# Optimization experiments

Measured on AMD Instinct MI355X. Metric: run time of the kernel, lower is better.

The kernel has to match this reference:

```python
import jax, jax.numpy as jnp
import numpy as np

NU, MS, DT, R = 128, 64, 128, 4
D_, K_, B_ = 10.0, 0.3, 0.3  # Layer1 sigmoid-gain hyperparams (LBKT defaults)


def setup_inputs() -> dict:
    key = jax.random.key(0)
    ks = jax.random.split(key, 16)
    B = 4096
    glorot = lambda k, shape: jax.random.normal(k, shape, jnp.float32) * np.sqrt(2.0 / (shape[-2] + shape[-1]))
    return {
        "inputs": jax.random.uniform(ks[0], (B, NU + MS + DT + 3), jnp.float32),
        "states": jax.random.normal(ks[1], (1, B, MS, NU), jnp.float32),
        "time_weight": glorot(ks[2], (R, NU + 1, NU)),
        "attempt_weight": glorot(ks[3], (R, NU + 1, NU)),
        "hint_weight": glorot(ks[4], (R, NU + 1, NU)),
        "Wf": glorot(ks[5], (1, R)),
        "bias": glorot(ks[6], (1, NU)),
        "gate3_W": glorot(ks[7], (2 * NU + 150, NU)),
        "gate3_b": jnp.zeros((NU,), jnp.float32),
        "out_W": glorot(ks[8], (NU + DT, NU)),
        "out_b": jnp.zeros((NU,), jnp.float32),
        "tg_W": glorot(ks[9], (2 * NU, NU)),
        "tg_b": jnp.zeros((1, NU), jnp.float32),
        "ag_W": glorot(ks[10], (2 * NU, NU)),
        "ag_b": jnp.zeros((1, NU), jnp.float32),
        "hg_W": glorot(ks[11], (2 * NU, NU)),
        "hg_b": jnp.zeros((1, NU), jnp.float32),
    }


def reference(inputs, states, time_weight, attempt_weight, hint_weight, Wf, bias,
              gate3_W, gate3_b, out_W, out_b, tg_W, tg_b, ag_W, ag_b, hg_W, hg_b):
    interact_emb = inputs[:, :NU]                       # (B, NU)
    corr = inputs[:, NU:NU + MS]                        # (B, MS) correlation weights
    topic = inputs[:, NU + MS:NU + MS + DT]             # (B, DT)
    t_f = inputs[:, -3:-2]                              # (B, 1)
    a_f = inputs[:, -2:-1]
    h_f = inputs[:, -1:]
    h_pre = states[0]                                   # (B, MS, NU)

    # correlation-weighted memory read
    h_pre_tilde = jnp.einsum('bm,bmn->bn', corr, h_pre)

    out_layer = lambda x: jax.nn.sigmoid(x @ out_W + out_b)
    preds = out_layer(jnp.concatenate([h_pre_tilde, topic], -1)).sum(-1, keepdims=True) / NU

    # Layer1 behavior-gain sub-networks: sigmoid(linear([h_tilde, interact]) * gain(factor))
    hx = jnp.concatenate([h_pre_tilde, interact_emb], -1)  # (B, 2*NU)
    def layer1(factor, W, b):
        gain = K_ + (1.0 - K_) / (1.0 + jnp.exp(-D_ * (factor - B_)))  # (B,1)
        return jax.nn.sigmoid((hx @ W + b) * gain)

    time_gain = layer1(t_f, tg_W, tg_b)
    attempt_gain = layer1(a_f, ag_W, ag_b)
    hint_gain = layer1(h_f, hg_W, hg_b)

    # low-rank tensor fusion: append a ones column, contract against (R, NU+1, NU)
    pad = jnp.ones_like(t_f)
    fuse = lambda g, W: jnp.einsum('bu,run->rbn', jnp.concatenate([g, pad], -1), W)
    fusion_all = fuse(time_gain, time_weight) * fuse(attempt_gain, attempt_weight) * fuse(hint_gain, hint_weight)
    fusion_all = jnp.einsum('or,rbn->bn', Wf, fusion_all) + bias  # (B, NU)
    learning_gain = jax.nn.relu(fusion_all)

    # outer-product write over memory slots
    LG = corr[:, :, None] * learning_gain[:, None, :]   # (B, MS, NU)

    Bsz = inputs.shape[0]
    tile50 = lambda f: jnp.broadcast_to(f[:, None, :], (Bsz, MS, 50))
    gate_in = jnp.concatenate([
        h_pre,
        jnp.broadcast_to(interact_emb[:, None, :], (Bsz, MS, NU)),
        tile50(t_f), tile50(a_f), tile50(h_f),
    ], -1)                                              # (B, MS, 2*NU+150)
    forget_gate = jax.nn.sigmoid(gate_in @ gate3_W + gate3_b)

    h = h_pre * forget_gate + LG                        # dropout inactive (inference)
    h_tilde = jnp.einsum('bm,bmn->bn', corr, h)
    after_preds = out_layer(jnp.concatenate([h_tilde, topic], -1)).sum(-1, keepdims=True) / NU
    improve = (after_preds - preds) / (1.0 - preds)
    result = jnp.concatenate([preds, improve], -1)      # (B, 2)
    return result, h
```

## Files before the change

### kernel.cpp

```cpp
#include <hip/hip_runtime.h>

#define B_TOT 4096
#define IN_W 323

typedef __attribute__((ext_vector_type(8))) short short8;
typedef __attribute__((ext_vector_type(4))) float f32x4;
typedef unsigned short ushort_t;

#define MFMA16(a, b, c) __builtin_amdgcn_mfma_f32_16x16x32_bf16(a, b, c, 0, 0, 0)

__device__ __forceinline__ float sigmoidf_(float x) { return 1.0f / (1.0f + __expf(-x)); }

__device__ __forceinline__ ushort_t f2bf(float f) {
    unsigned int u = __float_as_uint(f);
    u += 0x7FFF + ((u >> 16) & 1);
    return (ushort_t)(u >> 16);
}

union BF8 { ushort_t u[8]; short8 v; };

struct WS {
    ushort_t *hpt, *ieb, *topb, *gains, *htldb;
    ushort_t *oWb, *tgWb, *agWb, *hgWb, *g3W2b, *W1b, *fWb;
    float *wsum, *preds, *cvec, *lg;
};

__global__ __launch_bounds__(256) void k0_prep(
    const float* __restrict__ inp, const float* __restrict__ oW,
    const float* __restrict__ tgW, const float* __restrict__ agW, const float* __restrict__ hgW,
    const float* __restrict__ g3W, const float* __restrict__ tw, const float* __restrict__ aw,
    const float* __restrict__ hw, WS w) {
    int bx = blockIdx.x, tid = threadIdx.x;
    if (bx < 128) {
        int mat = bx >> 5, c = bx & 31;
        const float* src = mat == 0 ? oW : mat == 1 ? tgW : mat == 2 ? agW : hgW;
        ushort_t* dst = mat == 0 ? w.oWb : mat == 1 ? w.tgWb : mat == 2 ? w.agWb : w.hgWb;
        if (tid < 128) {
            int n = tid;
#pragma unroll
            for (int j = 0; j < 8; ++j)
                dst[(size_t)n * 256 + c * 8 + j] = f2bf(src[(size_t)(c * 8 + j) * 128 + n]);
        }
    } else if (bx < 352) {
        int i = bx - 128, mat = i >> 4, c = i & 15;
        const float* src;
        ushort_t* dst;
        if (mat == 0) { src = g3W + 128 * 128; dst = w.g3W2b; }
        else if (mat == 1) { src = g3W; dst = w.W1b; }
        else {
            int f = mat - 2, g = f >> 2, r = f & 3;
            const float* base = g == 0 ? tw : g == 1 ? aw : hw;
            src = base + (size_t)r * 129 * 128;
            dst = w.fWb + (size_t)f * 128 * 128;
        }
        if (tid < 128) {
            int n = tid;
#pragma unroll
            for (int j = 0; j < 8; ++j)
                dst[(size_t)n * 128 + c * 8 + j] = f2bf(src[(size_t)(c * 8 + j) * 128 + n]);
        }
    } else if (bx == 352) {
        if (tid < 128) {
            int n = tid;
            float st = 0.f, sa = 0.f, sh = 0.f;
            for (int k = 0; k < 50; ++k) {
                st += g3W[(size_t)(256 + k) * 128 + n];
                sa += g3W[(size_t)(306 + k) * 128 + n];
                sh += g3W[(size_t)(356 + k) * 128 + n];
            }
            w.wsum[n] = st; w.wsum[128 + n] = sa; w.wsum[256 + n] = sh;
        }
    } else {
        int id0 = (bx - 353) * 256 + tid;
        for (int id = id0; id < 2 * B_TOT * 128; id += 1024 * 256) {
            int arr = id >> 19;
            int rem = id & 524287;
            int b = rem >> 7, n = rem & 127;
            float v = inp[(size_t)b * IN_W + (arr ? 192 : 0) + n];
            (arr ? w.topb : w.ieb)[rem] = f2bf(v);
        }
    }
}

__global__ __launch_bounds__(256) void k1a_hpt(const float* __restrict__ inp,
                                               const float* __restrict__ hp, WS w) {
    __shared__ float s_corr[8][64];
    int tid = threadIdx.x, b0 = blockIdx.x * 8;
    for (int i = tid; i < 512; i += 256) {
        int bl = i >> 6, m = i & 63;
        s_corr[bl][m] = inp[(size_t)(b0 + bl) * IN_W + 128 + m];
    }
    __syncthreads();
    int bl = tid >> 5, c4 = (tid & 31) * 4;
    const float* hpb = hp + (size_t)(b0 + bl) * 8192 + c4;
    float a0 = 0, a1 = 0, a2 = 0, a3 = 0;
#pragma unroll 8
    for (int m = 0; m < 64; ++m) {
        float cr = s_corr[bl][m];
        float4 v = *(const float4*)(hpb + m * 128);
        a0 += cr * v.x; a1 += cr * v.y; a2 += cr * v.z; a3 += cr * v.w;
    }
    ushort_t* dst = w.hpt + (size_t)(b0 + bl) * 128 + c4;
    dst[0] = f2bf(a0); dst[1] = f2bf(a1); dst[2] = f2bf(a2); dst[3] = f2bf(a3);
}

__global__ __launch_bounds__(256) void k1b_gemms(
    const float* __restrict__ inp, const float* __restrict__ ob,
    const float* __restrict__ tgb, const float* __restrict__ agb, const float* __restrict__ hgb,
    const float* __restrict__ g3b, WS w) {
    __shared__ float s_red[4][16];
    int tid = threadIdx.x;
    int job = blockIdx.y;
    int m0 = blockIdx.x * 16;
    int wv = tid >> 6, l = tid & 63;
    int lr = l & 15, lg_ = l >> 4;
    int ncol0 = wv * 32;
    const ushort_t* Bw = job == 0 ? w.oWb : job == 1 ? w.tgWb : job == 2 ? w.agWb
                         : job == 3 ? w.hgWb : w.g3W2b;
    const int K = (job == 4) ? 128 : 256;
    f32x4 acc0 = {0, 0, 0, 0}, acc1 = {0, 0, 0, 0};
    for (int k0 = 0; k0 < K; k0 += 32) {
        const ushort_t* Ab;
        int ka;
        if (job == 4) { Ab = w.ieb; ka = k0; }
        else if (k0 < 128) { Ab = w.hpt; ka = k0; }
        else { Ab = (job == 0) ? w.topb : w.ieb; ka = k0 - 128; }
        short8 a = *(const short8*)(Ab + (size_t)(m0 + lr) * 128 + ka + lg_ * 8);
        short8 b0v = *(const short8*)(Bw + (size_t)(ncol0 + lr) * K + k0 + lg_ * 8);
        short8 b1v = *(const short8*)(Bw + (size_t)(ncol0 + 16 + lr) * K + k0 + lg_ * 8);
        acc0 = MFMA16(a, b0v, acc0);
        acc1 = MFMA16(a, b1v, acc1);
    }
    if (job == 0) {
        float s[4];
#pragma unroll
        for (int rr = 0; rr < 4; ++rr)
            s[rr] = sigmoidf_(acc0[rr] + ob[ncol0 + lr]) + sigmoidf_(acc1[rr] + ob[ncol0 + 16 + lr]);
#pragma unroll
        for (int off = 1; off <= 8; off <<= 1)
#pragma unroll
            for (int rr = 0; rr < 4; ++rr) s[rr] += __shfl_xor(s[rr], off);
        if (lr == 0)
#pragma unroll
            for (int rr = 0; rr < 4; ++rr) s_red[wv][lg_ * 4 + rr] = s[rr];
        __syncthreads();
        if (tid < 16) {
            float p = (s_red[0][tid] + s_red[1][tid] + s_red[2][tid] + s_red[3][tid]) * (1.f / 128.f);
            w.preds[m0 + tid] = p;
        }
    } else if (job <= 3) {
        const float* gb = job == 1 ? tgb : job == 2 ? agb : hgb;
        ushort_t* gout = w.gains + (size_t)(job - 1) * B_TOT * 128;
#pragma unroll
        for (int half = 0; half < 2; ++half) {
            f32x4 acc = half ? acc1 : acc0;
            int n = ncol0 + half * 16 + lr;
            float gbn = gb[n];
#pragma unroll
            for (int rr = 0; rr < 4; ++rr) {
                int b = m0 + lg_ * 4 + rr;
                float f = inp[(size_t)b * IN_W + 320 + (job - 1)];
                float gf = 0.3f + 0.7f * sigmoidf_(10.f * (f - 0.3f));
                gout[(size_t)b * 128 + n] = f2bf(sigmoidf_((acc[rr] + gbn) * gf));
            }
        }
    } else {
#pragma unroll
        for (int half = 0; half < 2; ++half) {
            f32x4 acc = half ? acc1 : acc0;
            int n = ncol0 + half * 16 + lr;
            float wst = w.wsum[n], wsa = w.wsum[128 + n], wsh = w.wsum[256 + n];
            float gbn = g3b[n];
#pragma unroll
            for (int rr = 0; rr < 4; ++rr) {
                int b = m0 + lg_ * 4 + rr;
                const float* sp = inp + (size_t)b * IN_W + 320;
                w.cvec[(size_t)b * 128 + n] = acc[rr] + sp[0] * wst + sp[1] * wsa + sp[2] * wsh + gbn;
            }
        }
    }
}

__global__ __launch_bounds__(512) void k1c_fusion(
    const float* __restrict__ tw, const float* __restrict__ aw, const float* __restrict__ hw,
    const float* __restrict__ wf, const float* __restrict__ bias, WS w) {
    __shared__ float s_red[4][16][128];
    int tid = threadIdx.x;
    int m0 = blockIdx.x * 16;
    int wv = tid >> 6, l = tid & 63;
    int r = wv >> 1, nh = wv & 1;
    int lr = l & 15, lg_ = l >> 4;
    f32x4 acc[3][4];
#pragma unroll
    for (int g = 0; g < 3; ++g)
#pragma unroll
        for (int nt = 0; nt < 4; ++nt) acc[g][nt] = (f32x4){0, 0, 0, 0};
#pragma unroll
    for (int g = 0; g < 3; ++g) {
        const ushort_t* Ag = w.gains + (size_t)g * B_TOT * 128;
        const ushort_t* Bg = w.fWb + (size_t)(g * 4 + r) * 128 * 128;
#pragma unroll
        for (int k0 = 0; k0 < 128; k0 += 32) {
            short8 a = *(const short8*)(Ag + (size_t)(m0 + lr) * 128 + k0 + lg_ * 8);
#pragma unroll
            for (int nt = 0; nt < 4; ++nt) {
                short8 b = *(const short8*)(Bg + (size_t)(nh * 64 + nt * 16 + lr) * 128 + k0 + lg_ * 8);
                acc[g][nt] = MFMA16(a, b, acc[g][nt]);
            }
        }
    }
    float wfr = wf[r];
    const float* pad0 = tw + (size_t)(r * 129 + 128) * 128;
    const float* pad1 = aw + (size_t)(r * 129 + 128) * 128;
    const float* pad2 = hw + (size_t)(r * 129 + 128) * 128;
#pragma unroll
    for (int nt = 0; nt < 4; ++nt) {
        int n = nh * 64 + nt * 16 + lr;
        float p0 = pad0[n], p1 = pad1[n], p2 = pad2[n];
#pragma unroll
        for (int rr = 0; rr < 4; ++rr) {
            float F0 = acc[0][nt][rr] + p0;
            float F1 = acc[1][nt][rr] + p1;
            float F2 = acc[2][nt][rr] + p2;
            s_red[r][lg_ * 4 + rr][n] = wfr * F0 * F1 * F2;
        }
    }
    __syncthreads();
    for (int i = tid; i < 2048; i += 512) {
        int row = i >> 7, col = i & 127;
        float v = s_red[0][row][col] + s_red[1][row][col] + s_red[2][row][col] + s_red[3][row][col];
        w.lg[(size_t)(m0 + row) * 128 + col] = fmaxf(v + bias[col], 0.f);
    }
}

__global__ __launch_bounds__(256) void k2_big(const float* __restrict__ inp,
                                              const float* __restrict__ hp, WS w,
                                              float* __restrict__ out_h) {
    __shared__ __align__(16) ushort_t s_w1[128 * 136];
    __shared__ float s_corr[64], s_lg[128], s_cv[128], s_ht[4][128];
    int tid = threadIdx.x, b = blockIdx.x;
    for (int i = tid; i < 128 * 16; i += 256) {
        int row = i >> 4, c8 = (i & 15) * 8;
        *(short8*)(s_w1 + row * 136 + c8) = *(const short8*)(w.W1b + (size_t)row * 128 + c8);
    }
    if (tid < 64) s_corr[tid] = inp[(size_t)b * IN_W + 128 + tid];
    if (tid < 128) s_lg[tid] = w.lg[(size_t)b * 128 + tid];
    else if (tid < 256) { int t = tid - 128; s_cv[t] = w.cvec[(size_t)b * 128 + t]; }
    __syncthreads();
    int wv = tid >> 6, l = tid & 63;
    int lr = l & 15, lg_ = l >> 4;
    int m0 = wv * 16;
    const float* hpb = hp + (size_t)b * 8192;
    short8 afr[4];
#pragma unroll
    for (int k0i = 0; k0i < 4; ++k0i) {
        const float* p = hpb + (m0 + lr) * 128 + k0i * 32 + lg_ * 8;
        float4 x0 = *(const float4*)p, x1 = *(const float4*)(p + 4);
        BF8 t;
        t.u[0] = f2bf(x0.x); t.u[1] = f2bf(x0.y); t.u[2] = f2bf(x0.z); t.u[3] = f2bf(x0.w);
        t.u[4] = f2bf(x1.x); t.u[5] = f2bf(x1.y); t.u[6] = f2bf(x1.z); t.u[7] = f2bf(x1.w);
        afr[k0i] = t.v;
    }
    float* outb = out_h + (size_t)b * 8192;
#pragma unroll
    for (int nt = 0; nt < 8; ++nt) {
        f32x4 acc = {0, 0, 0, 0};
#pragma unroll
        for (int k0i = 0; k0i < 4; ++k0i) {
            short8 bv = *(const short8*)(s_w1 + (nt * 16 + lr) * 136 + k0i * 32 + lg_ * 8);
            acc = MFMA16(afr[k0i], bv, acc);
        }
        int n = nt * 16 + lr;
        float cv = s_cv[n], lgv = s_lg[n];
        float csum = 0.f;
#pragma unroll
        for (int rr = 0; rr < 4; ++rr) {
            int m = m0 + lg_ * 4 + rr;
            float fg = sigmoidf_(acc[rr] + cv);
            float hpv = hpb[m * 128 + n];
            float cr = s_corr[m];
            float hv = hpv * fg + cr * lgv;
            outb[m * 128 + n] = hv;
            csum += cr * hv;
        }
        csum += __shfl_xor(csum, 16);
        csum += __shfl_xor(csum, 32);
        if (l < 16) s_ht[wv][n] = csum;
    }
    __syncthreads();
    if (tid < 128) {
        float s = s_ht[0][tid] + s_ht[1][tid] + s_ht[2][tid] + s_ht[3][tid];
        w.htldb[(size_t)b * 128 + tid] = f2bf(s);
    }
}

__global__ __launch_bounds__(256) void k3_after(const float* __restrict__ ob, WS w,
                                               float* __restrict__ out_res) {
    __shared__ float s_red[4][16];
    int tid = threadIdx.x, m0 = blockIdx.x * 16;
    int wv = tid >> 6, l = tid & 63, lr = l & 15, lg_ = l >> 4;
    int ncol0 = wv * 32;
    f32x4 acc0 = {0, 0, 0, 0}, acc1 = {0, 0, 0, 0};
    for (int k0 = 0; k0 < 256; k0 += 32) {
        const ushort_t* Ab = (k0 < 128) ? w.htldb : w.topb;
        int ka = k0 & 127;
        short8 a = *(const short8*)(Ab + (size_t)(m0 + lr) * 128 + ka + lg_ * 8);
        short8 b0v = *(const short8*)(w.oWb + (size_t)(ncol0 + lr) * 256 + k0 + lg_ * 8);
        short8 b1v = *(const short8*)(w.oWb + (size_t)(ncol0 + 16 + lr) * 256 + k0 + lg_ * 8);
        acc0 = MFMA16(a, b0v, acc0);
        acc1 = MFMA16(a, b1v, acc1);
    }
    float s[4];
#pragma unroll
    for (int rr = 0; rr < 4; ++rr)
        s[rr] = sigmoidf_(acc0[rr] + ob[ncol0 + lr]) + sigmoidf_(acc1[rr] + ob[ncol0 + 16 + lr]);
#pragma unroll
    for (int off = 1; off <= 8; off <<= 1)
#pragma unroll
        for (int rr = 0; rr < 4; ++rr) s[rr] += __shfl_xor(s[rr], off);
    if (lr == 0)
#pragma unroll
        for (int rr = 0; rr < 4; ++rr) s_red[wv][lg_ * 4 + rr] = s[rr];
    __syncthreads();
    if (tid < 16) {
        float ap = (s_red[0][tid] + s_red[1][tid] + s_red[2][tid] + s_red[3][tid]) * (1.f / 128.f);
        float p = w.preds[m0 + tid];
        out_res[(size_t)(m0 + tid) * 2] = p;
        out_res[(size_t)(m0 + tid) * 2 + 1] = (ap - p) / (1.f - p);
    }
}

extern "C" void kernel_launch(void* const* d_in, const int* in_sizes, int n_in,
                              void* d_out, int out_size, void* d_ws, size_t ws_size,
                              hipStream_t stream) {
    const float* inp  = (const float*)d_in[0];
    const float* st   = (const float*)d_in[1];
    const float* tw   = (const float*)d_in[2];
    const float* aw   = (const float*)d_in[3];
    const float* hw   = (const float*)d_in[4];
    const float* wf   = (const float*)d_in[5];
    const float* bias = (const float*)d_in[6];
    const float* g3W  = (const float*)d_in[7];
    const float* g3b  = (const float*)d_in[8];
    const float* oW   = (const float*)d_in[9];
    const float* ob   = (const float*)d_in[10];
    const float* tgW  = (const float*)d_in[11];
    const float* tgb  = (const float*)d_in[12];
    const float* agW  = (const float*)d_in[13];
    const float* agb  = (const float*)d_in[14];
    const float* hgW  = (const float*)d_in[15];
    const float* hgb  = (const float*)d_in[16];

    float* out_res = (float*)d_out;
    float* out_h   = (float*)d_out + 2 * B_TOT;

    char* p = (char*)d_ws;
    auto alloc = [&](size_t bytes) { char* r = p; p += (bytes + 255) & ~255ull; return r; };
    WS w;
    w.hpt   = (ushort_t*)alloc((size_t)B_TOT * 128 * 2);
    w.ieb   = (ushort_t*)alloc((size_t)B_TOT * 128 * 2);
    w.topb  = (ushort_t*)alloc((size_t)B_TOT * 128 * 2);
    w.gains = (ushort_t*)alloc((size_t)3 * B_TOT * 128 * 2);
    w.htldb = (ushort_t*)alloc((size_t)B_TOT * 128 * 2);
    w.oWb   = (ushort_t*)alloc(256 * 128 * 2);
    w.tgWb  = (ushort_t*)alloc(256 * 128 * 2);
    w.agWb  = (ushort_t*)alloc(256 * 128 * 2);
    w.hgWb  = (ushort_t*)alloc(256 * 128 * 2);
    w.g3W2b = (ushort_t*)alloc(128 * 128 * 2);
    w.W1b   = (ushort_t*)alloc(128 * 128 * 2);
    w.fWb   = (ushort_t*)alloc(12 * 128 * 128 * 2);
    w.wsum  = (float*)alloc(3 * 128 * 4);
    w.preds = (float*)alloc(B_TOT * 4);
    w.cvec  = (float*)alloc((size_t)B_TOT * 128 * 4);
    w.lg    = (float*)alloc((size_t)B_TOT * 128 * 4);

    k0_prep<<<1377, 256, 0, stream>>>(inp, oW, tgW, agW, hgW, g3W, tw, aw, hw, w);
    k1a_hpt<<<B_TOT / 8, 256, 0, stream>>>(inp, st, w);
    k1b_gemms<<<dim3(B_TOT / 16, 5), 256, 0, stream>>>(inp, ob, tgb, agb, hgb, g3b, w);
    k1c_fusion<<<B_TOT / 16, 512, 0, stream>>>(tw, aw, hw, wf, bias, w);
    k2_big<<<B_TOT, 256, 0, stream>>>(inp, st, w, out_h);
    k3_after<<<B_TOT / 16, 256, 0, stream>>>(ob, w, out_res);
}
```

Measured before the change: 356.1 us.

## Fuse stage-one kernels into one block-local pass and batch memory-update blocks

Merges the memory read, the gain/pred/gate GEMMs and the fusion GEMM into a single kernel. Intermediates (h_tilde, embeddings, gains) now stay in shared memory instead of round-tripping through global bf16 buffers. The weight prep kernel now transposes through shared memory with coalesced loads. The big update kernel processes four samples per block, one per wave, so the W1 tile staged in shared memory is reused across samples. The after kernel converts topic values from the inputs inline. The trade-off is fewer, heavier blocks with more serial MFMA work per wave and higher shared-memory use.

```diff
diff --git a/kernel.cpp b/kernel.cpp
--- a/kernel.cpp
+++ b/kernel.cpp
@@ -5,61 +5,32 @@
 
 typedef __attribute__((ext_vector_type(8))) short short8;
 typedef __attribute__((ext_vector_type(4))) float f32x4;
-typedef unsigned short ushort_t;
+typedef unsigned short u16;
 
 #define MFMA16(a, b, c) __builtin_amdgcn_mfma_f32_16x16x32_bf16(a, b, c, 0, 0, 0)
 
 __device__ __forceinline__ float sigmoidf_(float x) { return 1.0f / (1.0f + __expf(-x)); }
 
-__device__ __forceinline__ ushort_t f2bf(float f) {
+__device__ __forceinline__ u16 f2bf(float f) {
     unsigned int u = __float_as_uint(f);
     u += 0x7FFF + ((u >> 16) & 1);
-    return (ushort_t)(u >> 16);
-}
-
-union BF8 { ushort_t u[8]; short8 v; };
+    return (u16)(u >> 16);
+}
+
+union BF8 { u16 u[8]; short8 v; };
 
 struct WS {
-    ushort_t *hpt, *ieb, *topb, *gains, *htldb;
-    ushort_t *oWb, *tgWb, *agWb, *hgWb, *g3W2b, *W1b, *fWb;
+    u16 *oWb, *tgWb, *agWb, *hgWb, *g3W2b, *W1b, *fWb, *htldb;
     float *wsum, *preds, *cvec, *lg;
 };
 
 __global__ __launch_bounds__(256) void k0_prep(
-    const float* __restrict__ inp, const float* __restrict__ oW,
-    const float* __restrict__ tgW, const float* __restrict__ agW, const float* __restrict__ hgW,
-    const float* __restrict__ g3W, const float* __restrict__ tw, const float* __restrict__ aw,
-    const float* __restrict__ hw, WS w) {
+    const float* __restrict__ oW, const float* __restrict__ tgW,
+    const float* __restrict__ agW, const float* __restrict__ hgW,
+    const float* __restrict__ g3W, const float* __restrict__ tw,
+    const float* __restrict__ aw, const float* __restrict__ hw, WS w) {
     int bx = blockIdx.x, tid = threadIdx.x;
-    if (bx < 128) {
-        int mat = bx >> 5, c = bx & 31;
-        const float* src = mat == 0 ? oW : mat == 1 ? tgW : mat == 2 ? agW : hgW;
-        ushort_t* dst = mat == 0 ? w.oWb : mat == 1 ? w.tgWb : mat == 2 ? w.agWb : w.hgWb;
-        if (tid < 128) {
-            int n = tid;
-#pragma unroll
-            for (int j = 0; j < 8; ++j)
-                dst[(size_t)n * 256 + c * 8 + j] = f2bf(src[(size_t)(c * 8 + j) * 128 + n]);
-        }
-    } else if (bx < 352) {
-        int i = bx - 128, mat = i >> 4, c = i & 15;
-        const float* src;
-        ushort_t* dst;
-        if (mat == 0) { src = g3W + 128 * 128; dst = w.g3W2b; }
-        else if (mat == 1) { src = g3W; dst = w.W1b; }
-        else {
-            int f = mat - 2, g = f >> 2, r = f & 3;
-            const float* base = g == 0 ? tw : g == 1 ? aw : hw;
-            src = base + (size_t)r * 129 * 128;
-            dst = w.fWb + (size_t)f * 128 * 128;
-        }
-        if (tid < 128) {
-            int n = tid;
-#pragma unroll
-            for (int j = 0; j < 8; ++j)
-                dst[(size_t)n * 128 + c * 8 + j] = f2bf(src[(size_t)(c * 8 + j) * 128 + n]);
-        }
-    } else if (bx == 352) {
+    if (bx == 88) {
         if (tid < 128) {
             int n = tid;
             float st = 0.f, sa = 0.f, sh = 0.f;
@@ -70,72 +41,105 @@
             }
             w.wsum[n] = st; w.wsum[128 + n] = sa; w.wsum[256 + n] = sh;
         }
+        return;
+    }
+    __shared__ float s_t[32][132];
+    const float* src; u16* dst; int K, k0;
+    if (bx < 32) {
+        int mat = bx >> 3; k0 = (bx & 7) * 32; K = 256;
+        src = mat == 0 ? oW : mat == 1 ? tgW : mat == 2 ? agW : hgW;
+        dst = mat == 0 ? w.oWb : mat == 1 ? w.tgWb : mat == 2 ? w.agWb : w.hgWb;
     } else {
-        int id0 = (bx - 353) * 256 + tid;
-        for (int id = id0; id < 2 * B_TOT * 128; id += 1024 * 256) {
-            int arr = id >> 19;
-            int rem = id & 524287;
-            int b = rem >> 7, n = rem & 127;
-            float v = inp[(size_t)b * IN_W + (arr ? 192 : 0) + n];
-            (arr ? w.topb : w.ieb)[rem] = f2bf(v);
-        }
-    }
-}
-
-__global__ __launch_bounds__(256) void k1a_hpt(const float* __restrict__ inp,
-                                               const float* __restrict__ hp, WS w) {
-    __shared__ float s_corr[8][64];
-    int tid = threadIdx.x, b0 = blockIdx.x * 8;
-    for (int i = tid; i < 512; i += 256) {
+        int i = bx - 32; int mat = i >> 2; k0 = (i & 3) * 32; K = 128;
+        if (mat == 0) { src = g3W; dst = w.W1b; }
+        else if (mat == 1) { src = g3W + 128 * 128; dst = w.g3W2b; }
+        else {
+            int f = mat - 2, g = f >> 2, r = f & 3;
+            src = (g == 0 ? tw : g == 1 ? aw : hw) + (size_t)r * 129 * 128;
+            dst = w.fWb + (size_t)f * 128 * 128;
+        }
+    }
+#pragma unroll
+    for (int jj = 0; jj < 4; ++jj) {
+        int id = tid + jj * 256;
+        int row = id >> 5, c4 = (id & 31) * 4;
+        float4 v = *(const float4*)(src + (size_t)(k0 + row) * 128 + c4);
+        s_t[row][c4] = v.x; s_t[row][c4 + 1] = v.y;
+        s_t[row][c4 + 2] = v.z; s_t[row][c4 + 3] = v.w;
+    }
+    __syncthreads();
+    int n = tid >> 1, half = (tid & 1) * 16;
+#pragma unroll
+    for (int j = 0; j < 16; ++j)
+        dst[(size_t)n * K + k0 + half + j] = f2bf(s_t[half + j][n]);
+}
+
+__global__ __launch_bounds__(512) void kA_stage(
+    const float* __restrict__ inp, const float* __restrict__ hp,
+    const float* __restrict__ ob, const float* __restrict__ tgb,
+    const float* __restrict__ agb, const float* __restrict__ hgb,
+    const float* __restrict__ g3b, const float* __restrict__ tw,
+    const float* __restrict__ aw, const float* __restrict__ hw,
+    const float* __restrict__ wf, const float* __restrict__ bias, WS w) {
+    __shared__ __align__(16) u16 s_hpt[16][136], s_ie[16][136], s_top[16][136];
+    __shared__ __align__(16) u16 s_g[3][16][136];
+    __shared__ float s_corr[16][64];
+    __shared__ float s_scal[16][4];
+    __shared__ float s_red[8][16];
+
+    int tid = threadIdx.x;
+    int b0 = blockIdx.x * 16;
+
+    for (int i = tid; i < 1024; i += 512) {
         int bl = i >> 6, m = i & 63;
         s_corr[bl][m] = inp[(size_t)(b0 + bl) * IN_W + 128 + m];
     }
-    __syncthreads();
-    int bl = tid >> 5, c4 = (tid & 31) * 4;
-    const float* hpb = hp + (size_t)(b0 + bl) * 8192 + c4;
-    float a0 = 0, a1 = 0, a2 = 0, a3 = 0;
+    {
+        int bl = tid >> 5, c4 = (tid & 31) * 4;
+        const float* row = inp + (size_t)(b0 + bl) * IN_W;
+#pragma unroll
+        for (int j = 0; j < 4; ++j) s_ie[bl][c4 + j] = f2bf(row[c4 + j]);
+#pragma unroll
+        for (int j = 0; j < 4; ++j) s_top[bl][c4 + j] = f2bf(row[192 + c4 + j]);
+    }
+    if (tid < 64) {
+        int bl = tid >> 2, j = tid & 3;
+        if (j < 3) s_scal[bl][j] = inp[(size_t)(b0 + bl) * IN_W + 320 + j];
+    }
+    __syncthreads();
+
+    {
+        int bl = tid >> 5, c4 = (tid & 31) * 4;
+        const float* hpb = hp + (size_t)(b0 + bl) * 8192 + c4;
+        float a0 = 0, a1 = 0, a2 = 0, a3 = 0;
 #pragma unroll 8
-    for (int m = 0; m < 64; ++m) {
-        float cr = s_corr[bl][m];
-        float4 v = *(const float4*)(hpb + m * 128);
-        a0 += cr * v.x; a1 += cr * v.y; a2 += cr * v.z; a3 += cr * v.w;
-    }
-    ushort_t* dst = w.hpt + (size_t)(b0 + bl) * 128 + c4;
-    dst[0] = f2bf(a0); dst[1] = f2bf(a1); dst[2] = f2bf(a2); dst[3] = f2bf(a3);
-}
-
-__global__ __launch_bounds__(256) void k1b_gemms(
-    const float* __restrict__ inp, const float* __restrict__ ob,
-    const float* __restrict__ tgb, const float* __restrict__ agb, const float* __restrict__ hgb,
-    const float* __restrict__ g3b, WS w) {
-    __shared__ float s_red[4][16];
-    int tid = threadIdx.x;
-    int job = blockIdx.y;
-    int m0 = blockIdx.x * 16;
-    int wv = tid >> 6, l = tid & 63;
-    int lr = l & 15, lg_ = l >> 4;
-    int ncol0 = wv * 32;
-    const ushort_t* Bw = job == 0 ? w.oWb : job == 1 ? w.tgWb : job == 2 ? w.agWb
-                         : job == 3 ? w.hgWb : w.g3W2b;
-    const int K = (job == 4) ? 128 : 256;
-    f32x4 acc0 = {0, 0, 0, 0}, acc1 = {0, 0, 0, 0};
-    for (int k0 = 0; k0 < K; k0 += 32) {
-        const ushort_t* Ab;
-        int ka;
-        if (job == 4) { Ab = w.ieb; ka = k0; }
-        else if (k0 < 128) { Ab = w.hpt; ka = k0; }
-        else { Ab = (job == 0) ? w.topb : w.ieb; ka = k0 - 128; }
-        short8 a = *(const short8*)(Ab + (size_t)(m0 + lr) * 128 + ka + lg_ * 8);
-        short8 b0v = *(const short8*)(Bw + (size_t)(ncol0 + lr) * K + k0 + lg_ * 8);
-        short8 b1v = *(const short8*)(Bw + (size_t)(ncol0 + 16 + lr) * K + k0 + lg_ * 8);
-        acc0 = MFMA16(a, b0v, acc0);
-        acc1 = MFMA16(a, b1v, acc1);
-    }
-    if (job == 0) {
+        for (int m = 0; m < 64; ++m) {
+            float cr = s_corr[bl][m];
+            float4 v = *(const float4*)(hpb + m * 128);
+            a0 += cr * v.x; a1 += cr * v.y; a2 += cr * v.z; a3 += cr * v.w;
+        }
+        s_hpt[bl][c4] = f2bf(a0); s_hpt[bl][c4 + 1] = f2bf(a1);
+        s_hpt[bl][c4 + 2] = f2bf(a2); s_hpt[bl][c4 + 3] = f2bf(a3);
+    }
+    __syncthreads();
+
+    int wv = tid >> 6, l = tid & 63, lr = l & 15, lg_ = l >> 4;
+    int n = wv * 16 + lr;
+
+    {
+        f32x4 acc = {0.f, 0.f, 0.f, 0.f};
+#pragma unroll
+        for (int k0 = 0; k0 < 256; k0 += 32) {
+            const u16* Ar = (k0 < 128) ? &s_hpt[lr][k0 + lg_ * 8]
+                                       : &s_top[lr][(k0 - 128) + lg_ * 8];
+            short8 a = *(const short8*)Ar;
+            short8 b = *(const short8*)(w.oWb + (size_t)n * 256 + k0 + lg_ * 8);
+            acc = MFMA16(a, b, acc);
+        }
+        float obn = ob[n];
         float s[4];
 #pragma unroll
-        for (int rr = 0; rr < 4; ++rr)
-            s[rr] = sigmoidf_(acc0[rr] + ob[ncol0 + lr]) + sigmoidf_(acc1[rr] + ob[ncol0 + 16 + lr]);
+        for (int rr = 0; rr < 4; ++rr) s[rr] = sigmoidf_(acc[rr] + obn);
 #pragma unroll
         for (int off = 1; off <= 8; off <<= 1)
 #pragma unroll
@@ -143,168 +147,178 @@
         if (lr == 0)
 #pragma unroll
             for (int rr = 0; rr < 4; ++rr) s_red[wv][lg_ * 4 + rr] = s[rr];
-        __syncthreads();
-        if (tid < 16) {
-            float p = (s_red[0][tid] + s_red[1][tid] + s_red[2][tid] + s_red[3][tid]) * (1.f / 128.f);
-            w.preds[m0 + tid] = p;
-        }
-    } else if (job <= 3) {
-        const float* gb = job == 1 ? tgb : job == 2 ? agb : hgb;
-        ushort_t* gout = w.gains + (size_t)(job - 1) * B_TOT * 128;
-#pragma unroll
-        for (int half = 0; half < 2; ++half) {
-            f32x4 acc = half ? acc1 : acc0;
-            int n = ncol0 + half * 16 + lr;
-            float gbn = gb[n];
+    }
+
+    {
+        const float* GB[3] = {tgb, agb, hgb};
+        const u16* GW[3] = {w.tgWb, w.agWb, w.hgWb};
+#pragma unroll
+        for (int g = 0; g < 3; ++g) {
+            f32x4 acc = {0.f, 0.f, 0.f, 0.f};
+#pragma unroll
+            for (int k0 = 0; k0 < 256; k0 += 32) {
+                const u16* Ar = (k0 < 128) ? &s_hpt[lr][k0 + lg_ * 8]
+                                           : &s_ie[lr][(k0 - 128) + lg_ * 8];
+                short8 a = *(const short8*)Ar;
+                short8 b = *(const short8*)(GW[g] + (size_t)n * 256 + k0 + lg_ * 8);
+                acc = MFMA16(a, b, acc);
+            }
+            float gbn = GB[g][n];
 #pragma unroll
             for (int rr = 0; rr < 4; ++rr) {
-                int b = m0 + lg_ * 4 + rr;
-                float f = inp[(size_t)b * IN_W + 320 + (job - 1)];
-                float gf = 0.3f + 0.7f * sigmoidf_(10.f * (f - 0.3f));
-                gout[(size_t)b * 128 + n] = f2bf(sigmoidf_((acc[rr] + gbn) * gf));
-            }
-        }
-    } else {
-#pragma unroll
-        for (int half = 0; half < 2; ++half) {
-            f32x4 acc = half ? acc1 : acc0;
-            int n = ncol0 + half * 16 + lr;
-            float wst = w.wsum[n], wsa = w.wsum[128 + n], wsh = w.wsum[256 + n];
-            float gbn = g3b[n];
-#pragma unroll
-            for (int rr = 0; rr < 4; ++rr) {
-                int b = m0 + lg_ * 4 + rr;
-                const float* sp = inp + (size_t)b * IN_W + 320;
-                w.cvec[(size_t)b * 128 + n] = acc[rr] + sp[0] * wst + sp[1] * wsa + sp[2] * wsh + gbn;
-            }
-        }
-    }
-}
-
-__global__ __launch_bounds__(512) void k1c_fusion(
-    const float* __restrict__ tw, const float* __restrict__ aw, const float* __restrict__ hw,
-    const float* __restrict__ wf, const float* __restrict__ bias, WS w) {
-    __shared__ float s_red[4][16][128];
-    int tid = threadIdx.x;
-    int m0 = blockIdx.x * 16;
-    int wv = tid >> 6, l = tid & 63;
-    int r = wv >> 1, nh = wv & 1;
-    int lr = l & 15, lg_ = l >> 4;
-    f32x4 acc[3][4];
-#pragma unroll
-    for (int g = 0; g < 3; ++g)
-#pragma unroll
-        for (int nt = 0; nt < 4; ++nt) acc[g][nt] = (f32x4){0, 0, 0, 0};
-#pragma unroll
-    for (int g = 0; g < 3; ++g) {
-        const ushort_t* Ag = w.gains + (size_t)g * B_TOT * 128;
-        const ushort_t* Bg = w.fWb + (size_t)(g * 4 + r) * 128 * 128;
+                int bl = lg_ * 4 + rr;
+                float gf = 0.3f + 0.7f * sigmoidf_(10.f * (s_scal[bl][g] - 0.3f));
+                s_g[g][bl][n] = f2bf(sigmoidf_((acc[rr] + gbn) * gf));
+            }
+        }
+    }
+
+    {
+        f32x4 acc = {0.f, 0.f, 0.f, 0.f};
 #pragma unroll
         for (int k0 = 0; k0 < 128; k0 += 32) {
-            short8 a = *(const short8*)(Ag + (size_t)(m0 + lr) * 128 + k0 + lg_ * 8);
-#pragma unroll
-            for (int nt = 0; nt < 4; ++nt) {
-                short8 b = *(const short8*)(Bg + (size_t)(nh * 64 + nt * 16 + lr) * 128 + k0 + lg_ * 8);
-                acc[g][nt] = MFMA16(a, b, acc[g][nt]);
-            }
-        }
-    }
-    float wfr = wf[r];
-    const float* pad0 = tw + (size_t)(r * 129 + 128) * 128;
-    const float* pad1 = aw + (size_t)(r * 129 + 128) * 128;
-    const float* pad2 = hw + (size_t)(r * 129 + 128) * 128;
-#pragma unroll
-    for (int nt = 0; nt < 4; ++nt) {
-        int n = nh * 64 + nt * 16 + lr;
-        float p0 = pad0[n], p1 = pad1[n], p2 = pad2[n];
+            short8 a = *(const short8*)&s_ie[lr][k0 + lg_ * 8];
+            short8 b = *(const short8*)(w.g3W2b + (size_t)n * 128 + k0 + lg_ * 8);
+            acc = MFMA16(a, b, acc);
+        }
+        float wst = w.wsum[n], wsa = w.wsum[128 + n], wsh = w.wsum[256 + n];
+        float gbn = g3b[n];
 #pragma unroll
         for (int rr = 0; rr < 4; ++rr) {
-            float F0 = acc[0][nt][rr] + p0;
-            float F1 = acc[1][nt][rr] + p1;
-            float F2 = acc[2][nt][rr] + p2;
-            s_red[r][lg_ * 4 + rr][n] = wfr * F0 * F1 * F2;
-        }
-    }
-    __syncthreads();
-    for (int i = tid; i < 2048; i += 512) {
-        int row = i >> 7, col = i & 127;
-        float v = s_red[0][row][col] + s_red[1][row][col] + s_red[2][row][col] + s_red[3][row][col];
-        w.lg[(size_t)(m0 + row) * 128 + col] = fmaxf(v + bias[col], 0.f);
+            int bl = lg_ * 4 + rr;
+            w.cvec[(size_t)(b0 + bl) * 128 + n] =
+                acc[rr] + s_scal[bl][0] * wst + s_scal[bl][1] * wsa + s_scal[bl][2] * wsh + gbn;
+        }
+    }
+    __syncthreads();
+
+    {
+        float lgacc[4] = {0.f, 0.f, 0.f, 0.f};
+#pragma unroll
+        for (int r = 0; r < 4; ++r) {
+            f32x4 F[3];
+#pragma unroll
+            for (int g = 0; g < 3; ++g) {
+                f32x4 acc = {0.f, 0.f, 0.f, 0.f};
+                const u16* Bg = w.fWb + (size_t)(g * 4 + r) * 16384;
+#pragma unroll
+                for (int k0 = 0; k0 < 128; k0 += 32) {
+                    short8 a = *(const short8*)&s_g[g][lr][k0 + lg_ * 8];
+                    short8 b = *(const short8*)(Bg + (size_t)n * 128 + k0 + lg_ * 8);
+                    acc = MFMA16(a, b, acc);
+                }
+                const float* pad = (g == 0 ? tw : g == 1 ? aw : hw) + (size_t)(r * 129 + 128) * 128;
+                float pv = pad[n];
+#pragma unroll
+                for (int rr = 0; rr < 4; ++rr) F[g][rr] = acc[rr] + pv;
+            }
+            float wfr = wf[r];
+#pragma unroll
+            for (int rr = 0; rr < 4; ++rr) lgacc[rr] += wfr * F[0][rr] * F[1][rr] * F[2][rr];
+        }
+        float bn = bias[n];
+#pragma unroll
+        for (int rr = 0; rr < 4; ++rr)
+            w.lg[(size_t)(b0 + lg_ * 4 + rr) * 128 + n] = fmaxf(lgacc[rr] + bn, 0.f);
+    }
+
+    if (tid < 16) {
+        float p = 0.f;
+#pragma unroll
+        for (int q = 0; q < 8; ++q) p += s_red[q][tid];
+        w.preds[b0 + tid] = p * (1.f / 128.f);
     }
 }
 
 __global__ __launch_bounds__(256) void k2_big(const float* __restrict__ inp,
                                               const float* __restrict__ hp, WS w,
                                               float* __restrict__ out_h) {
-    __shared__ __align__(16) ushort_t s_w1[128 * 136];
-    __shared__ float s_corr[64], s_lg[128], s_cv[128], s_ht[4][128];
-    int tid = threadIdx.x, b = blockIdx.x;
-    for (int i = tid; i < 128 * 16; i += 256) {
+    __shared__ __align__(16) u16 s_w1[128 * 136];
+    __shared__ float s_lg[4][128], s_cv[4][128], s_corr[4][64];
+    int tid = threadIdx.x, b0 = blockIdx.x * 4;
+    for (int i = tid; i < 2048; i += 256) {
         int row = i >> 4, c8 = (i & 15) * 8;
         *(short8*)(s_w1 + row * 136 + c8) = *(const short8*)(w.W1b + (size_t)row * 128 + c8);
     }
-    if (tid < 64) s_corr[tid] = inp[(size_t)b * IN_W + 128 + tid];
-    if (tid < 128) s_lg[tid] = w.lg[(size_t)b * 128 + tid];
-    else if (tid < 256) { int t = tid - 128; s_cv[t] = w.cvec[(size_t)b * 128 + t]; }
-    __syncthreads();
-    int wv = tid >> 6, l = tid & 63;
-    int lr = l & 15, lg_ = l >> 4;
-    int m0 = wv * 16;
+    for (int i = tid; i < 512; i += 256) {
+        int bl = i >> 7, c = i & 127;
+        s_lg[bl][c] = w.lg[(size_t)(b0 + bl) * 128 + c];
+        s_cv[bl][c] = w.cvec[(size_t)(b0 + bl) * 128 + c];
+    }
+    {
+        int bl = tid >> 6, m = tid & 63;
+        s_corr[bl][m] = inp[(size_t)(b0 + bl) * IN_W + 128 + m];
+    }
+    __syncthreads();
+
+    int wv = tid >> 6, l = tid & 63, lr = l & 15, lg_ = l >> 4;
+    int b = b0 + wv;
     const float* hpb = hp + (size_t)b * 8192;
-    short8 afr[4];
-#pragma unroll
-    for (int k0i = 0; k0i < 4; ++k0i) {
-        const float* p = hpb + (m0 + lr) * 128 + k0i * 32 + lg_ * 8;
-        float4 x0 = *(const float4*)p, x1 = *(const float4*)(p + 4);
-        BF8 t;
-        t.u[0] = f2bf(x0.x); t.u[1] = f2bf(x0.y); t.u[2] = f2bf(x0.z); t.u[3] = f2bf(x0.w);
-        t.u[4] = f2bf(x1.x); t.u[5] = f2bf(x1.y); t.u[6] = f2bf(x1.z); t.u[7] = f2bf(x1.w);
-        afr[k0i] = t.v;
-    }
     float* outb = out_h + (size_t)b * 8192;
+    float csum[8] = {0.f, 0.f, 0.f, 0.f, 0.f, 0.f, 0.f, 0.f};
+
+#pragma unroll
+    for (int mt = 0; mt < 4; ++mt) {
+        short8 afr[4];
+#pragma unroll
+        for (int k0i = 0; k0i < 4; ++k0i) {
+            const float* p = hpb + (mt * 16 + lr) * 128 + k0i * 32 + lg_ * 8;
+            float4 x0 = *(const float4*)p, x1 = *(const float4*)(p + 4);
+            BF8 t;
+            t.u[0] = f2bf(x0.x); t.u[1] = f2bf(x0.y); t.u[2] = f2bf(x0.z); t.u[3] = f2bf(x0.w);
+            t.u[4] = f2bf(x1.x); t.u[5] = f2bf(x1.y); t.u[6] = f2bf(x1.z); t.u[7] = f2bf(x1.w);
+            afr[k0i] = t.v;
+        }
+#pragma unroll
+        for (int nt = 0; nt < 8; ++nt) {
+            f32x4 acc = {0.f, 0.f, 0.f, 0.f};
+#pragma unroll
+            for (int k0i = 0; k0i < 4; ++k0i) {
+                short8 bv = *(const short8*)(s_w1 + (nt * 16 + lr) * 136 + k0i * 32 + lg_ * 8);
+                acc = MFMA16(afr[k0i], bv, acc);
+            }
+            int n = nt * 16 + lr;
+            float cv = s_cv[wv][n], lgv = s_lg[wv][n];
+#pragma unroll
+            for (int rr = 0; rr < 4; ++rr) {
+                int m = mt * 16 + lg_ * 4 + rr;
+                float cr = s_corr[wv][m];
+                float fg = sigmoidf_(acc[rr] + cv);
+                float hv = hpb[m * 128 + n] * fg + cr * lgv;
+                outb[m * 128 + n] = hv;
+                csum[nt] += cr * hv;
+            }
+        }
+    }
 #pragma unroll
     for (int nt = 0; nt < 8; ++nt) {
-        f32x4 acc = {0, 0, 0, 0};
-#pragma unroll
-        for (int k0i = 0; k0i < 4; ++k0i) {
-            short8 bv = *(const short8*)(s_w1 + (nt * 16 + lr) * 136 + k0i * 32 + lg_ * 8);
-            acc = MFMA16(afr[k0i], bv, acc);
-        }
-        int n = nt * 16 + lr;
-        float cv = s_cv[n], lgv = s_lg[n];
-        float csum = 0.f;
-#pragma unroll
-        for (int rr = 0; rr < 4; ++rr) {
-            int m = m0 + lg_ * 4 + rr;
-            float fg = sigmoidf_(acc[rr] + cv);
-            float hpv = hpb[m * 128 + n];
-            float cr = s_corr[m];
-            float hv = hpv * fg + cr * lgv;
-            outb[m * 128 + n] = hv;
-            csum += cr * hv;
-        }
-        csum += __shfl_xor(csum, 16);
-        csum += __shfl_xor(csum, 32);
-        if (l < 16) s_ht[wv][n] = csum;
-    }
-    __syncthreads();
-    if (tid < 128) {
-        float s = s_ht[0][tid] + s_ht[1][tid] + s_ht[2][tid] + s_ht[3][tid];
-        w.htldb[(size_t)b * 128 + tid] = f2bf(s);
-    }
-}
-
-__global__ __launch_bounds__(256) void k3_after(const float* __restrict__ ob, WS w,
-                                               float* __restrict__ out_res) {
+        float c = csum[nt];
+        c += __shfl_xor(c, 16);
+        c += __shfl_xor(c, 32);
+        if (l < 16) w.htldb[(size_t)b * 128 + nt * 16 + l] = f2bf(c);
+    }
+}
+
+__global__ __launch_bounds__(256) void k3_after(const float* __restrict__ inp,
+                                                const float* __restrict__ ob, WS w,
+                                                float* __restrict__ out_res) {
     __shared__ float s_red[4][16];
     int tid = threadIdx.x, m0 = blockIdx.x * 16;
     int wv = tid >> 6, l = tid & 63, lr = l & 15, lg_ = l >> 4;
     int ncol0 = wv * 32;
-    f32x4 acc0 = {0, 0, 0, 0}, acc1 = {0, 0, 0, 0};
+    f32x4 acc0 = {0.f, 0.f, 0.f, 0.f}, acc1 = {0.f, 0.f, 0.f, 0.f};
+#pragma unroll
     for (int k0 = 0; k0 < 256; k0 += 32) {
-        const ushort_t* Ab = (k0 < 128) ? w.htldb : w.topb;
-        int ka = k0 & 127;
-        short8 a = *(const short8*)(Ab + (size_t)(m0 + lr) * 128 + ka + lg_ * 8);
+        short8 a;
+        if (k0 < 128) {
+            a = *(const short8*)(w.htldb + (size_t)(m0 + lr) * 128 + k0 + lg_ * 8);
+        } else {
+            const float* p = inp + (size_t)(m0 + lr) * IN_W + 192 + (k0 - 128) + lg_ * 8;
+            BF8 t;
+#pragma unroll
+            for (int j = 0; j < 8; ++j) t.u[j] = f2bf(p[j]);
+            a = t.v;
+        }
         short8 b0v = *(const short8*)(w.oWb + (size_t)(ncol0 + lr) * 256 + k0 + lg_ * 8);
         short8 b1v = *(const short8*)(w.oWb + (size_t)(ncol0 + 16 + lr) * 256 + k0 + lg_ * 8);
         acc0 = MFMA16(a, b0v, acc0);
@@ -357,27 +371,22 @@
     char* p = (char*)d_ws;
     auto alloc = [&](size_t bytes) { char* r = p; p += (bytes + 255) & ~255ull; return r; };
     WS w;
-    w.hpt   = (ushort_t*)alloc((size_t)B_TOT * 128 * 2);
-    w.ieb   = (ushort_t*)alloc((size_t)B_TOT * 128 * 2);
-    w.topb  = (ushort_t*)alloc((size_t)B_TOT * 128 * 2);
-    w.gains = (ushort_t*)alloc((size_t)3 * B_TOT * 128 * 2);
-    w.htldb = (ushort_t*)alloc((size_t)B_TOT * 128 * 2);
-    w.oWb   = (ushort_t*)alloc(256 * 128 * 2);
-    w.tgWb  = (ushort_t*)alloc(256 * 128 * 2);
-    w.agWb  = (ushort_t*)alloc(256 * 128 * 2);
-    w.hgWb  = (ushort_t*)alloc(256 * 128 * 2);
-    w.g3W2b = (ushort_t*)alloc(128 * 128 * 2);
-    w.W1b   = (ushort_t*)alloc(128 * 128 * 2);
-    w.fWb   = (ushort_t*)alloc(12 * 128 * 128 * 2);
+    w.oWb   = (u16*)alloc(256 * 128 * 2);
+    w.tgWb  = (u16*)alloc(256 * 128 * 2);
+    w.agWb  = (u16*)alloc(256 * 128 * 2);
+    w.hgWb  = (u16*)alloc(256 * 128 * 2);
+    w.g3W2b = (u16*)alloc(128 * 128 * 2);
+    w.W1b   = (u16*)alloc(128 * 128 * 2);
+    w.fWb   = (u16*)alloc(12 * 128 * 128 * 2);
+    w.htldb = (u16*)alloc((size_t)B_TOT * 128 * 2);
     w.wsum  = (float*)alloc(3 * 128 * 4);
     w.preds = (float*)alloc(B_TOT * 4);
     w.cvec  = (float*)alloc((size_t)B_TOT * 128 * 4);
     w.lg    = (float*)alloc((size_t)B_TOT * 128 * 4);
 
-    k0_prep<<<1377, 256, 0, stream>>>(inp, oW, tgW, agW, hgW, g3W, tw, aw, hw, w);
-    k1a_hpt<<<B_TOT / 8, 256, 0, stream>>>(inp, st, w);
-    k1b_gemms<<<dim3(B_TOT / 16, 5), 256, 0, stream>>>(inp, ob, tgb, agb, hgb, g3b, w);
-    k1c_fusion<<<B_TOT / 16, 512, 0, stream>>>(tw, aw, hw, wf, bias, w);
-    k2_big<<<B_TOT, 256, 0, stream>>>(inp, st, w, out_h);
-    k3_after<<<B_TOT / 16, 256, 0, stream>>>(ob, w, out_res);
-}
+    k0_prep<<<89, 256, 0, stream>>>(oW, tgW, agW, hgW, g3W, tw, aw, hw, w);
+    kA_stage<<<B_TOT / 16, 512, 0, stream>>>(inp, st, ob, tgb, agb, hgb, g3b,
+                                             tw, aw, hw, wf, bias, w);
+    k2_big<<<B_TOT / 4, 256, 0, stream>>>(inp, st, w, out_h);
+    k3_after<<<B_TOT / 16, 256, 0, stream>>>(inp, ob, w, out_res);
+}
```

After: 389.1 us. +9.3%, slower.
